# Kernel optimization log

Measured on AMD Instinct MI355X. Metric: run time of the kernel, lower is better.

The kernel has to match this reference:

```python
import jax, jax.numpy as jnp
import numpy as np

IN_F = 4096
OUT_F = 11008
GROUP = 128
BATCH = 32
Q_OUT = OUT_F // 2          # two int4 values packed per byte along out dim
N_GROUPS = IN_F // GROUP    # 32 groups


def setup_inputs() -> dict:
    key = jax.random.key(0)
    k1, k2, k3, k4, k5 = jax.random.split(key, 5)
    inp = jax.random.normal(k1, (BATCH, 1, IN_F), dtype=jnp.float32)
    qweight = jax.random.randint(k2, (IN_F, Q_OUT), 0, 256, dtype=jnp.int32)   # packed bytes
    scales = jax.random.uniform(k3, (N_GROUPS, OUT_F), dtype=jnp.float32) * 0.01
    qzeros = jax.random.randint(k4, (N_GROUPS, Q_OUT), 0, 256, dtype=jnp.int32)  # packed bytes
    bias = jax.random.normal(k5, (OUT_F,), dtype=jnp.float32)
    return {"input": inp, "qweight": qweight, "scales": scales, "qzeros": qzeros, "bias": bias}


def _unpack_int4(packed, n_out):
    # packed: [rows, n_out//2] bytes; low nibble -> even out col, high nibble -> odd out col
    low = packed & 0xF
    high = (packed >> 4) & 0xF
    return jnp.stack([low, high], axis=-1).reshape(packed.shape[0], n_out)


def reference(input, qweight, scales, qzeros, bias):
    # GPTQ-style grouped dequant: w[k, n] = (q[k, n] - zero[g(k), n]) * scale[g(k), n]
    q = _unpack_int4(qweight, OUT_F).astype(jnp.float32)   # [K, N]
    z = _unpack_int4(qzeros, OUT_F).astype(jnp.float32)    # [G, N]
    gidx = jnp.arange(IN_F) // GROUP                       # [K] group index per input channel
    w = (q - z[gidx]) * scales[gidx]                       # [K, N] dequantized weight
    # decode GEMV/GEMM: [B, 1, K] x [K, N] -> [B, 1, N], plus bias (mm_bias_int4 path)
    return jnp.einsum('bsk,kn->bsn', input, w) + bias
```

## Files before the change

kernel.cpp:

```cpp
#include <hip/hip_runtime.h>
#include <hip/hip_fp16.h>
#include <cstdint>

#define IN_F 4096
#define OUT_F 11008
#define Q_OUT 5504
#define GROUP 128
#define BATCH 32

#define KBS 8
#define GPB 4
#define NCH 8
#define BN 64
#define BROWS 66

typedef _Float16 f16x8 __attribute__((ext_vector_type(8)));
typedef float    f32x4 __attribute__((ext_vector_type(4)));

__global__ __launch_bounds__(256)
void xprep_kernel(const float* __restrict__ x, uint4* __restrict__ xf)
{
    const int t    = blockIdx.x * 256 + threadIdx.x;
    const int lane = t & 63;
    const int f    = (t >> 6) & 1;
    const int S    = t >> 7;
    const int m    = f * 16 + (lane & 15);
    const int k0   = S * 32 + (lane >> 4) * 8;
    const float4* xr = reinterpret_cast<const float4*>(x + (size_t)m * IN_F + k0);
    float4 a = xr[0], b = xr[1];
    union { _Float16 h[8]; uint4 u; } v;
    v.h[0] = (_Float16)a.x; v.h[1] = (_Float16)a.y;
    v.h[2] = (_Float16)a.z; v.h[3] = (_Float16)a.w;
    v.h[4] = (_Float16)b.x; v.h[5] = (_Float16)b.y;
    v.h[6] = (_Float16)b.z; v.h[7] = (_Float16)b.w;
    xf[t] = v.u;
}

__global__ __launch_bounds__(256)
void int4_gemm_kernel(const uint4* __restrict__ xf,
                      const int*   __restrict__ qw,
                      const float* __restrict__ scales,
                      const int*   __restrict__ qz,
                      float*       __restrict__ partial)
{
    const int tid  = threadIdx.x;
    const int lane = tid & 63;
    const int wid  = tid >> 6;
    const int nb   = blockIdx.x;
    const int kb   = blockIdx.y;
    const int g0   = kb * GPB;
    const int k0b  = g0 * GROUP;

    __shared__ int b_lds[2][32 * BROWS];

    const int cl  = lane & 15;
    const int kg  = lane >> 4;
    const int w   = wid * 8 + (cl >> 1);
    const int shn = (cl & 1) * 4;

    const int n = nb * BN + wid * 16 + cl;
    uint    zmu[GPB];
    __half2 spk[GPB];
    #pragma unroll
    for (int g = 0; g < GPB; ++g) {
        const float s = scales[(size_t)(g0 + g) * OUT_F + n];
        const int   z = (qz[(size_t)(g0 + g) * Q_OUT + (n >> 1)] >> shn) & 15;
        spk[g] = __float2half2_rn(s);
        zmu[g] = 0x64006400u + (uint)z * 0x00010001u;
    }

    const int a8 = tid & 7;
    const int bk = tid >> 3;

    f32x4 acc[2] = {};
    uint4 A[2][4];
    uint4 b0r, b1r;

    auto LOADA = [&](int c, int buf) {
        const size_t base = (size_t)(k0b / 32 + c * 2) * 128;
        A[buf][0] = xf[base +   0 + lane];
        A[buf][1] = xf[base +  64 + lane];
        A[buf][2] = xf[base + 128 + lane];
        A[buf][3] = xf[base + 192 + lane];
    };
    auto LOADB = [&](int c) {
        const int kr = k0b + c * 64;
        b0r = *reinterpret_cast<const uint4*>(qw + (size_t)(kr + bk)      * Q_OUT + nb * 32 + a8 * 4);
        b1r = *reinterpret_cast<const uint4*>(qw + (size_t)(kr + bk + 32) * Q_OUT + nb * 32 + a8 * 4);
    };
    auto WLDS = [&](int buf) {
        int* p = b_lds[buf];
        p[(4 * a8 + 0) * BROWS + bk] = b0r.x;
        p[(4 * a8 + 1) * BROWS + bk] = b0r.y;
        p[(4 * a8 + 2) * BROWS + bk] = b0r.z;
        p[(4 * a8 + 3) * BROWS + bk] = b0r.w;
        p[(4 * a8 + 0) * BROWS + bk + 32] = b1r.x;
        p[(4 * a8 + 1) * BROWS + bk + 32] = b1r.y;
        p[(4 * a8 + 2) * BROWS + bk + 32] = b1r.z;
        p[(4 * a8 + 3) * BROWS + bk + 32] = b1r.w;
    };

    LOADA(0, 0);
    LOADB(0);
    WLDS(0);
    __syncthreads();

    #pragma unroll
    for (int c = 0; c < NCH; ++c) {
        const int cur = c & 1;
        if (c + 1 < NCH) { LOADA(c + 1, cur ^ 1); LOADB(c + 1); }

        const int     gl  = c >> 1;
        const __half2 zmh = __builtin_bit_cast(__half2, zmu[gl]);
        const __half2 sg  = spk[gl];

        #pragma unroll
        for (int s = 0; s < 2; ++s) {
            const int* bp = &b_lds[cur][w * BROWS + s * 32 + kg * 8];
            int2 q0 = *reinterpret_cast<const int2*>(bp + 0);
            int2 q1 = *reinterpret_cast<const int2*>(bp + 2);
            int2 q2 = *reinterpret_cast<const int2*>(bp + 4);
            int2 q3 = *reinterpret_cast<const int2*>(bp + 6);

            union { uint u[4]; f16x8 v; } bf;
            const int2 qq[4] = {q0, q1, q2, q3};
            #pragma unroll
            for (int t = 0; t < 4; ++t) {
                uint pr = __builtin_amdgcn_perm((uint)qq[t].y, (uint)qq[t].x, 0x0C040C00u);
                pr >>= shn;
                uint qk = (pr & 0x000F000Fu) | 0x64006400u;
                __half2 wv = __hmul2(__hsub2(__builtin_bit_cast(__half2, qk), zmh), sg);
                bf.u[t] = __builtin_bit_cast(uint, wv);
            }
            f16x8 af0 = __builtin_bit_cast(f16x8, A[cur][s * 2 + 0]);
            f16x8 af1 = __builtin_bit_cast(f16x8, A[cur][s * 2 + 1]);
            acc[0] = __builtin_amdgcn_mfma_f32_16x16x32_f16(af0, bf.v, acc[0], 0, 0, 0);
            acc[1] = __builtin_amdgcn_mfma_f32_16x16x32_f16(af1, bf.v, acc[1], 0, 0, 0);
        }

        if (c + 1 < NCH) WLDS(cur ^ 1);
        __syncthreads();
    }

    #pragma unroll
    for (int f = 0; f < 2; ++f) {
        const int m = f * 16 + kg * 4;
        float* pp = partial + ((size_t)(kb * BATCH + m)) * OUT_F + n;
        pp[0]                 = acc[f][0];
        pp[(size_t)OUT_F]     = acc[f][1];
        pp[(size_t)OUT_F * 2] = acc[f][2];
        pp[(size_t)OUT_F * 3] = acc[f][3];
    }
}

__global__ __launch_bounds__(256)
void reduce_bias_kernel(const float* __restrict__ partial,
                        const float* __restrict__ bias,
                        float* __restrict__ out)
{
    const int i4 = (blockIdx.x * 256 + threadIdx.x) * 4;
    const int n  = i4 % OUT_F;
    float4 s = *reinterpret_cast<const float4*>(bias + n);
    #pragma unroll
    for (int kb = 0; kb < KBS; ++kb) {
        float4 p = *reinterpret_cast<const float4*>(partial + (size_t)kb * BATCH * OUT_F + i4);
        s.x += p.x; s.y += p.y; s.z += p.z; s.w += p.w;
    }
    *reinterpret_cast<float4*>(out + i4) = s;
}

extern "C" void kernel_launch(void* const* d_in, const int* in_sizes, int n_in,
                              void* d_out, int out_size, void* d_ws, size_t ws_size,
                              hipStream_t stream)
{
    const float* inp    = (const float*)d_in[0];
    const int*   qw     = (const int*)d_in[1];
    const float* scales = (const float*)d_in[2];
    const int*   qz     = (const int*)d_in[3];
    const float* bias   = (const float*)d_in[4];
    float*       out    = (float*)d_out;

    const size_t XFB = (size_t)BATCH * IN_F * 2;
    uint4* xf      = (uint4*)d_ws;
    float* partial = (float*)((char*)d_ws + XFB);

    xprep_kernel<<<64, 256, 0, stream>>>(inp, xf);

    int4_gemm_kernel<<<dim3(OUT_F / BN, KBS), 256, 0, stream>>>(
        xf, qw, scales, qz, partial);

    reduce_bias_kernel<<<(BATCH * OUT_F) / 1024, 256, 0, stream>>>(partial, bias, out);
}
```

Baseline: 31.21 us.

## Stage activations into LDS via async global_load_lds and deepen weight prefetch

```diff
diff --git a/kernel.cpp b/kernel.cpp
--- a/kernel.cpp
+++ b/kernel.cpp
@@ -51,7 +51,8 @@
     const int g0   = kb * GPB;
     const int k0b  = g0 * GROUP;
 
-    __shared__ int b_lds[2][32 * BROWS];
+    __shared__ uint4 a_lds[NCH * 4 * 64];
+    __shared__ int   b_lds[2][32 * BROWS];
 
     const int cl  = lane & 15;
     const int kg  = lane >> 4;
@@ -69,50 +70,55 @@
         zmu[g] = 0x64006400u + (uint)z * 0x00010001u;
     }
 
+    {
+        const size_t gbase = (size_t)(k0b / 32) * 2 * 64;
+        #pragma unroll
+        for (int r = 0; r < 8; ++r) {
+            const uint4* gp = xf + gbase + (size_t)r * 256 + tid;
+            __builtin_amdgcn_global_load_lds(
+                (const __attribute__((address_space(1))) uint32_t*)gp,
+                (__attribute__((address_space(3))) uint32_t*)&a_lds[r * 256 + wid * 64],
+                16, 0, 0);
+        }
+    }
+
     const int a8 = tid & 7;
     const int bk = tid >> 3;
 
     f32x4 acc[2] = {};
-    uint4 A[2][4];
-    uint4 b0r, b1r;
-
-    auto LOADA = [&](int c, int buf) {
-        const size_t base = (size_t)(k0b / 32 + c * 2) * 128;
-        A[buf][0] = xf[base +   0 + lane];
-        A[buf][1] = xf[base +  64 + lane];
-        A[buf][2] = xf[base + 128 + lane];
-        A[buf][3] = xf[base + 192 + lane];
+    uint4 br0[2], br1[2];
+
+    auto LOADB = [&](int c, int set) {
+        const int kr = k0b + c * 64;
+        br0[set] = *reinterpret_cast<const uint4*>(qw + (size_t)(kr + bk)      * Q_OUT + nb * 32 + a8 * 4);
+        br1[set] = *reinterpret_cast<const uint4*>(qw + (size_t)(kr + bk + 32) * Q_OUT + nb * 32 + a8 * 4);
     };
-    auto LOADB = [&](int c) {
-        const int kr = k0b + c * 64;
-        b0r = *reinterpret_cast<const uint4*>(qw + (size_t)(kr + bk)      * Q_OUT + nb * 32 + a8 * 4);
-        b1r = *reinterpret_cast<const uint4*>(qw + (size_t)(kr + bk + 32) * Q_OUT + nb * 32 + a8 * 4);
+    auto WLDS = [&](int buf, int set) {
+        int* p = b_lds[buf];
+        p[(4 * a8 + 0) * BROWS + bk]      = br0[set].x;
+        p[(4 * a8 + 1) * BROWS + bk]      = br0[set].y;
+        p[(4 * a8 + 2) * BROWS + bk]      = br0[set].z;
+        p[(4 * a8 + 3) * BROWS + bk]      = br0[set].w;
+        p[(4 * a8 + 0) * BROWS + bk + 32] = br1[set].x;
+        p[(4 * a8 + 1) * BROWS + bk + 32] = br1[set].y;
+        p[(4 * a8 + 2) * BROWS + bk + 32] = br1[set].z;
+        p[(4 * a8 + 3) * BROWS + bk + 32] = br1[set].w;
     };
-    auto WLDS = [&](int buf) {
-        int* p = b_lds[buf];
-        p[(4 * a8 + 0) * BROWS + bk] = b0r.x;
-        p[(4 * a8 + 1) * BROWS + bk] = b0r.y;
-        p[(4 * a8 + 2) * BROWS + bk] = b0r.z;
-        p[(4 * a8 + 3) * BROWS + bk] = b0r.w;
-        p[(4 * a8 + 0) * BROWS + bk + 32] = b1r.x;
-        p[(4 * a8 + 1) * BROWS + bk + 32] = b1r.y;
-        p[(4 * a8 + 2) * BROWS + bk + 32] = b1r.z;
-        p[(4 * a8 + 3) * BROWS + bk + 32] = b1r.w;
-    };
-
-    LOADA(0, 0);
-    LOADB(0);
-    WLDS(0);
-    __syncthreads();
+
+    LOADB(0, 0);
+    LOADB(1, 1);
+    WLDS(0, 0);
+    asm volatile("s_waitcnt vmcnt(0) lgkmcnt(0)" ::: "memory");
+    __builtin_amdgcn_s_barrier();
+    asm volatile("" ::: "memory");
 
     #pragma unroll
     for (int c = 0; c < NCH; ++c) {
         const int cur = c & 1;
-        if (c + 1 < NCH) { LOADA(c + 1, cur ^ 1); LOADB(c + 1); }
-
-        const int     gl  = c >> 1;
-        const __half2 zmh = __builtin_bit_cast(__half2, zmu[gl]);
-        const __half2 sg  = spk[gl];
+        if (c + 2 < NCH) LOADB(c + 2, cur);
+
+        const __half2 zmh = __builtin_bit_cast(__half2, zmu[c >> 1]);
+        const __half2 sg  = spk[c >> 1];
 
         #pragma unroll
         for (int s = 0; s < 2; ++s) {
@@ -132,14 +138,20 @@
                 __half2 wv = __hmul2(__hsub2(__builtin_bit_cast(__half2, qk), zmh), sg);
                 bf.u[t] = __builtin_bit_cast(uint, wv);
             }
-            f16x8 af0 = __builtin_bit_cast(f16x8, A[cur][s * 2 + 0]);
-            f16x8 af1 = __builtin_bit_cast(f16x8, A[cur][s * 2 + 1]);
+            uint4 a0u = a_lds[(c * 4 + s * 2 + 0) * 64 + lane];
+            uint4 a1u = a_lds[(c * 4 + s * 2 + 1) * 64 + lane];
+            f16x8 af0 = __builtin_bit_cast(f16x8, a0u);
+            f16x8 af1 = __builtin_bit_cast(f16x8, a1u);
             acc[0] = __builtin_amdgcn_mfma_f32_16x16x32_f16(af0, bf.v, acc[0], 0, 0, 0);
             acc[1] = __builtin_amdgcn_mfma_f32_16x16x32_f16(af1, bf.v, acc[1], 0, 0, 0);
         }
 
-        if (c + 1 < NCH) WLDS(cur ^ 1);
-        __syncthreads();
+        if (c + 1 < NCH) {
+            WLDS(cur ^ 1, cur ^ 1);
+            asm volatile("s_waitcnt lgkmcnt(0)" ::: "memory");
+            __builtin_amdgcn_s_barrier();
+            asm volatile("" ::: "memory");
+        }
     }
 
     #pragma unroll
```

New measurement: 31.46 us. Within noise of the previous version (+0.8%).
